# Kernel tuning notes

Hardware: AMD Instinct MI355X
Metric: run time of the kernel (lower is better)

Reference implementation:

```python
import jax, jax.numpy as jnp
import numpy as np

N, M, C, CSKIP, K = 16384, 4096, 256, 128, 3
BIG = 1e10  # distance penalty for cross-batch pairs


def setup_inputs() -> dict:
    key = jax.random.key(0)
    ks = jax.random.split(key, 6)
    return {
        "x": jax.random.normal(ks[0], (M, C), jnp.float32),
        "pos": jax.random.normal(ks[1], (M, 3), jnp.float32),
        "batch": jnp.zeros((M,), jnp.int32),
        "x_skip": jax.random.normal(ks[2], (N, CSKIP), jnp.float32),
        "pos_skip": jax.random.normal(ks[3], (N, 3), jnp.float32),
        "batch_skip": jnp.zeros((N,), jnp.int32),
        "W1": jax.random.normal(ks[4], (C + CSKIP, 256), jnp.float32) * (1.0 / np.sqrt(C + CSKIP)),
        "b1": jnp.zeros((256,), jnp.float32),
        "W2": jax.random.normal(ks[5], (256, 256), jnp.float32) * (1.0 / np.sqrt(256)),
        "b2": jnp.zeros((256,), jnp.float32),
    }


def _knn_idx(pos, pos_skip, batch, batch_skip, k):
    # Squared distances via GEMM form: [N, M]
    a2 = jnp.sum(pos_skip * pos_skip, axis=-1, keepdims=True)      # [N,1]
    b2 = jnp.sum(pos * pos, axis=-1)[None, :]                       # [1,M]
    d2 = a2 + b2 - 2.0 * (pos_skip @ pos.T)                         # [N,M]
    d2 = jnp.where(batch_skip[:, None] != batch[None, :], BIG, d2)
    _, idx = jax.lax.top_k(-d2, k)                                  # [N,k]
    return idx


def reference(x, pos, batch, x_skip, pos_skip, batch_skip, W1, b1, W2, b2):
    idx = _knn_idx(pos, pos_skip, batch, batch_skip, K)             # [N,k] coarse neighbor ids
    # Exact squared dist recomputed from gathered positions (matches torch diff path)
    diff = pos_skip[:, None, :] - pos[idx]                          # [N,k,3]
    d2 = jnp.sum(diff * diff, axis=-1, keepdims=True)               # [N,k,1]
    w = 1.0 / (d2 + 1e-8)                                           # inverse-distance weights
    wsum = jnp.sum(w, axis=1, keepdims=True)                        # per-row scatter_add == sum over k
    w = w / (wsum + 1e-8)
    x_interp = jnp.sum(w * x[idx], axis=1)                          # [N,C]
    h = jnp.concatenate([x_interp, x_skip], axis=1)                 # [N,C+C']
    h = jax.nn.relu(h @ W1 + b1)
    h = jax.nn.relu(h @ W2 + b2)
    return h
```

## Files before the change

### kernel.cpp

```cpp
#include <hip/hip_runtime.h>

typedef float     f4   __attribute__((ext_vector_type(4)));
typedef float     f32x4 __attribute__((ext_vector_type(4)));
typedef _Float16  h8   __attribute__((ext_vector_type(8)));
typedef _Float16  h4   __attribute__((ext_vector_type(4)));
typedef int       i4   __attribute__((ext_vector_type(4)));

#define NQ   16384
#define MP   4096
#define CF   256
#define CSK  128
#define K1   384
#define HID  256
#define QB   16

__global__ __launch_bounds__(256) void wconv_kernel(
    const float* __restrict__ W1, const float* __restrict__ W2,
    _Float16* __restrict__ Wt1, _Float16* __restrict__ Wt2)
{
    const int i = blockIdx.x * 256 + threadIdx.x;
    if (i < K1 * HID) {
        const int k = i >> 8, n = i & 255;
        Wt1[(size_t)(k >> 5) * 8192 + ((k >> 3) & 3) * 2048 + n * 8 + (k & 7)]
            = (_Float16)W1[i];
    } else {
        const int i2 = i - K1 * HID;
        const int k = i2 >> 8, n = i2 & 255;
        Wt2[(size_t)(k >> 5) * 8192 + ((k >> 3) & 3) * 2048 + n * 8 + (k & 7)]
            = (_Float16)W2[i2];
    }
}

__global__ __launch_bounds__(256, 3) void fused_kernel(
    const float* __restrict__ pos,
    const float* __restrict__ pos_skip,
    const float* __restrict__ x,
    const float* __restrict__ x_skip,
    const _Float16* __restrict__ Wt1,
    const _Float16* __restrict__ Wt2,
    const float* __restrict__ b1,
    const float* __restrict__ b2,
    float* __restrict__ out)
{
    __shared__ __align__(16) char smem[51456];
    float* px = (float*)smem;
    float* py = (float*)(smem + 16384);
    float* pz = (float*)(smem + 32768);
    unsigned short (*ci)[48]    = (unsigned short (*)[48])(smem + 49152);
    unsigned short (*ci2)[8][3] = (unsigned short (*)[8][3])(smem + 50688);
    int   (*fidx)[3] = (int (*)[3])(smem + 49152);
    float (*fw)[3]   = (float (*)[3])(smem + 49344);
    _Float16 (*As)[392] = (_Float16 (*)[392])smem;
    _Float16 (*Hs)[264] = (_Float16 (*)[264])smem;

    const int tid = threadIdx.x;

    for (int j = tid; j < MP; j += 256) {
        px[j] = pos[3*j+0];
        py[j] = pos[3*j+1];
        pz[j] = pos[3*j+2];
    }
    __syncthreads();

    const int lane = tid & 63;
    const int wv   = tid >> 6;

    {
        float qx[4], qy[4], qz[4];
        #pragma unroll
        for (int k = 0; k < 4; k++) {
            const int q = blockIdx.x * QB + wv * 4 + k;
            qx[k] = pos_skip[3*q+0];
            qy[k] = pos_skip[3*q+1];
            qz[k] = pos_skip[3*q+2];
        }

        unsigned K0[4], K1v[4], K2[4];
        #pragma unroll
        for (int k = 0; k < 4; k++) { K0[k] = ~0u; K1v[k] = ~0u; K2[k] = ~0u; }

        #define EVAL(PX, PY, PZ, J)                                           \
            _Pragma("unroll")                                                 \
            for (int k = 0; k < 4; k++) {                                     \
                const float dx = qx[k] - (PX), dy = qy[k] - (PY),             \
                            dz = qz[k] - (PZ);                                \
                const float dd = fmaf(dx, dx, fmaf(dy, dy, dz * dz));         \
                const unsigned key = (__float_as_uint(dd) & 0xFFFFF000u) | (J);\
                const unsigned h0 = max(K0[k], key);                          \
                K0[k] = min(K0[k], key);                                      \
                const unsigned n1 = min(K1v[k], h0);                          \
                const unsigned h1 = max(K1v[k], h0);                          \
                K1v[k] = n1;                                                  \
                K2[k] = min(K2[k], h1);                                       \
            }

        float c0x = px[lane],       c1x = px[lane + 64],
              c2x = px[lane + 128], c3x = px[lane + 192];
        float c0y = py[lane],       c1y = py[lane + 64],
              c2y = py[lane + 128], c3y = py[lane + 192];
        float c0z = pz[lane],       c1z = pz[lane + 64],
              c2z = pz[lane + 128], c3z = pz[lane + 192];

        for (int it = 0; it < 64; it += 4) {
            const unsigned jb = it * 64 + lane;
            const float nx0 = px[jb + 256], nx1 = px[jb + 320],
                        nx2 = px[jb + 384], nx3 = px[jb + 448];
            const float ny0 = py[jb + 256], ny1 = py[jb + 320],
                        ny2 = py[jb + 384], ny3 = py[jb + 448];
            const float nz0 = pz[jb + 256], nz1 = pz[jb + 320],
                        nz2 = pz[jb + 384], nz3 = pz[jb + 448];
            EVAL(c0x, c0y, c0z, jb);
            EVAL(c1x, c1y, c1z, jb + 64);
            EVAL(c2x, c2y, c2z, jb + 128);
            EVAL(c3x, c3y, c3z, jb + 192);
            c0x = nx0; c1x = nx1; c2x = nx2; c3x = nx3;
            c0y = ny0; c1y = ny1; c2y = ny2; c3y = ny3;
            c0z = nz0; c1z = nz1; c2z = nz2; c3z = nz3;
        }
        #undef EVAL

        #pragma unroll
        for (int k = 0; k < 4; k++) {
            unsigned a0 = K0[k], a1 = K1v[k], a2 = K2[k];
            {
                const unsigned b0 = (unsigned)__builtin_amdgcn_ds_swizzle((int)a0, 0x041F);
                const unsigned b1 = (unsigned)__builtin_amdgcn_ds_swizzle((int)a1, 0x041F);
                const unsigned b2 = (unsigned)__builtin_amdgcn_ds_swizzle((int)a2, 0x041F);
                const unsigned m0 = min(a0, b0);
                const unsigned c1 = max(a0, b0);
                const unsigned d0 = min(a1, b1), d1 = max(a1, b1);
                const unsigned m1 = min(c1, d0);
                const unsigned m2 = min(min(max(c1, d0), d1), min(a2, b2));
                a0 = m0; a1 = m1; a2 = m2;
            }
            {
                const unsigned b0 = (unsigned)__builtin_amdgcn_ds_swizzle((int)a0, 0x081F);
                const unsigned b1 = (unsigned)__builtin_amdgcn_ds_swizzle((int)a1, 0x081F);
                const unsigned b2 = (unsigned)__builtin_amdgcn_ds_swizzle((int)a2, 0x081F);
                const unsigned m0 = min(a0, b0);
                const unsigned c1 = max(a0, b0);
                const unsigned d0 = min(a1, b1), d1 = max(a1, b1);
                const unsigned m1 = min(c1, d0);
                const unsigned m2 = min(min(max(c1, d0), d1), min(a2, b2));
                a0 = m0; a1 = m1; a2 = m2;
            }
            if (!(lane & 3)) {
                const int q = wv * 4 + k;
                const int pr = lane >> 2;
                ci[q][pr*3+0] = (unsigned short)(a0 & 0xFFFu);
                ci[q][pr*3+1] = (unsigned short)(a1 & 0xFFFu);
                ci[q][pr*3+2] = (unsigned short)(a2 & 0xFFFu);
            }
        }
    }
    __syncthreads();

    if (tid < 8 * QB) {
        const int q    = tid >> 3;
        const int part = tid & 7;
        const int g    = blockIdx.x * QB + q;
        const double qxd = (double)pos_skip[3*g+0];
        const double qyd = (double)pos_skip[3*g+1];
        const double qzd = (double)pos_skip[3*g+2];
        const double a2d = qxd*qxd + qyd*qyd + qzd*qzd;

        double e0 = 1e300, e1 = 1e300, e2 = 1e300;
        int    j0 = 0,     j1 = 0,     j2 = 0;
        #pragma unroll
        for (int c = 0; c < 6; c++) {
            const int j = ci[q][part*6 + c];
            const double pxd = (double)px[j], pyd = (double)py[j],
                         pzd = (double)pz[j];
            const double b2  = pxd*pxd + pyd*pyd + pzd*pzd;
            const double dot = qxd*pxd + qyd*pyd + qzd*pzd;
            const double d   = (a2d + b2) - 2.0 * dot;
            if (d < e2) {
                if (d < e1) {
                    e2 = e1; j2 = j1;
                    if (d < e0) { e1 = e0; j1 = j0; e0 = d; j0 = j; }
                    else        { e1 = d;  j1 = j; }
                } else { e2 = d; j2 = j; }
            }
        }
        ci2[q][part][0] = (unsigned short)j0;
        ci2[q][part][1] = (unsigned short)j1;
        ci2[q][part][2] = (unsigned short)j2;
    }
    __syncthreads();

    if (tid < QB) {
        const int g = blockIdx.x * QB + tid;
        const double qxd = (double)pos_skip[3*g+0];
        const double qyd = (double)pos_skip[3*g+1];
        const double qzd = (double)pos_skip[3*g+2];
        const double a2d = qxd*qxd + qyd*qyd + qzd*qzd;

        double e0 = 1e300, e1 = 1e300, e2 = 1e300;
        int    j0 = 0,     j1 = 0,     j2 = 0;
        for (int p = 0; p < 8; p++) {
            #pragma unroll
            for (int s = 0; s < 3; s++) {
                const int j = ci2[tid][p][s];
                const double pxd = (double)px[j], pyd = (double)py[j],
                             pzd = (double)pz[j];
                const double b2  = pxd*pxd + pyd*pyd + pzd*pzd;
                const double dot = qxd*pxd + qyd*pyd + qzd*pzd;
                const double d   = (a2d + b2) - 2.0 * dot;
                if (d < e2) {
                    if (d < e1) {
                        e2 = e1; j2 = j1;
                        if (d < e0) { e1 = e0; j1 = j0; e0 = d; j0 = j; }
                        else        { e1 = d;  j1 = j; }
                    } else { e2 = d; j2 = j; }
                }
            }
        }
        const float sx = pos_skip[3*g+0], sy = pos_skip[3*g+1], sz = pos_skip[3*g+2];
        const int jj[3] = { j0, j1, j2 };
        float wv3[3];
        #pragma unroll
        for (int k = 0; k < 3; k++) {
            const float dx = sx - px[jj[k]], dy = sy - py[jj[k]],
                        dz = sz - pz[jj[k]];
            const float dd = dx*dx + dy*dy + dz*dz;
            wv3[k] = 1.0f / (dd + 1e-8f);
        }
        const float inv = 1.0f / (wv3[0] + wv3[1] + wv3[2] + 1e-8f);
        #pragma unroll
        for (int k = 0; k < 3; k++) {
            fidx[tid][k] = jj[k];
            fw[tid][k]   = wv3[k] * inv;
        }
    }
    __syncthreads();

    const int row0 = blockIdx.x * QB;

    {
        const int r   = tid >> 4;
        const int sub = tid & 15;
        const int j0 = fidx[r][0], j1 = fidx[r][1], j2 = fidx[r][2];
        const float w0 = fw[r][0], w1 = fw[r][1], w2 = fw[r][2];
        const f4* xa = (const f4*)(x + (size_t)j0 * CF);
        const f4* xb = (const f4*)(x + (size_t)j1 * CF);
        const f4* xc = (const f4*)(x + (size_t)j2 * CF);
        const f4* xs = (const f4*)(x_skip + (size_t)(row0 + r) * CSK);
        #pragma unroll
        for (int t = 0; t < 4; t++) {
            const int c4 = t * 16 + sub;
            const f4 a = xa[c4], b = xb[c4], c = xc[c4];
            const f4 v = a * w0 + b * w1 + c * w2;
            h4 hv; hv[0]=(_Float16)v[0]; hv[1]=(_Float16)v[1];
                   hv[2]=(_Float16)v[2]; hv[3]=(_Float16)v[3];
            *(h4*)&As[r][c4 * 4] = hv;
        }
        #pragma unroll
        for (int t = 0; t < 2; t++) {
            const int c4 = t * 16 + sub;
            const f4 v = xs[c4];
            h4 hv; hv[0]=(_Float16)v[0]; hv[1]=(_Float16)v[1];
                   hv[2]=(_Float16)v[2]; hv[3]=(_Float16)v[3];
            *(h4*)&As[r][CF + c4 * 4] = hv;
        }
    }

    const int ln   = tid & 15;
    const int quad = (tid >> 4) & 3;
    const int nb   = wv * 64;
    const int q8   = quad * 8;

    const _Float16* w1b = Wt1 + quad * 2048 + (size_t)(nb + ln) * 8;
    const _Float16* w2b = Wt2 + quad * 2048 + (size_t)(nb + ln) * 8;

    f32x4 acc[4];
    #pragma unroll
    for (int nt = 0; nt < 4; nt++) acc[nt] = (f32x4)0.0f;

    h8 B[6][4];
    #pragma unroll
    for (int s = 0; s < 6; s++)
        #pragma unroll
        for (int nt = 0; nt < 4; nt++)
            B[s][nt] = *(const h8*)(w1b + (size_t)s * 8192 + nt * 128);

    __syncthreads();

    #pragma unroll
    for (int kb = 0; kb < 12; kb++) {
        const int s = kb % 6;
        const h8 ha = *(const h8*)&As[ln][kb*32 + q8];
        h8 hb[4];
        #pragma unroll
        for (int nt = 0; nt < 4; nt++) hb[nt] = B[s][nt];
        if (kb < 6) {
            #pragma unroll
            for (int nt = 0; nt < 4; nt++)
                B[s][nt] = *(const h8*)(w1b + (size_t)(kb+6) * 8192 + nt * 128);
        } else {
            #pragma unroll
            for (int nt = 0; nt < 4; nt++)
                B[s][nt] = *(const h8*)(w2b + (size_t)(kb-6) * 8192 + nt * 128);
        }
        #pragma unroll
        for (int nt = 0; nt < 4; nt++)
            acc[nt] = __builtin_amdgcn_mfma_f32_16x16x32_f16(ha, hb[nt], acc[nt], 0, 0, 0);
    }
    __syncthreads();

    #pragma unroll
    for (int nt = 0; nt < 4; nt++) {
        const int n = nb + nt*16 + ln;
        const float bv = b1[n];
        #pragma unroll
        for (int r = 0; r < 4; r++) {
            const int m = quad*4 + r;
            Hs[m][n] = (_Float16)fmaxf(acc[nt][r] + bv, 0.0f);
        }
        acc[nt] = (f32x4)0.0f;
    }
    __syncthreads();

    #pragma unroll
    for (int kb = 0; kb < 8; kb++) {
        const int s = kb % 6;
        const h8 ha = *(const h8*)&Hs[ln][kb*32 + q8];
        h8 hb[4];
        #pragma unroll
        for (int nt = 0; nt < 4; nt++) hb[nt] = B[s][nt];
        if (kb < 2) {
            #pragma unroll
            for (int nt = 0; nt < 4; nt++)
                B[s][nt] = *(const h8*)(w2b + (size_t)(kb+6) * 8192 + nt * 128);
        }
        #pragma unroll
        for (int nt = 0; nt < 4; nt++)
            acc[nt] = __builtin_amdgcn_mfma_f32_16x16x32_f16(ha, hb[nt], acc[nt], 0, 0, 0);
    }

    #pragma unroll
    for (int nt = 0; nt < 4; nt++) {
        const int n = nb + nt*16 + ln;
        const float bv = b2[n];
        #pragma unroll
        for (int r = 0; r < 4; r++) {
            const int m = quad*4 + r;
            out[(size_t)(row0 + m) * HID + n] = fmaxf(acc[nt][r] + bv, 0.0f);
        }
    }
}

extern "C" void kernel_launch(void* const* d_in, const int* in_sizes, int n_in,
                              void* d_out, int out_size, void* d_ws, size_t ws_size,
                              hipStream_t stream) {
    const float* x         = (const float*)d_in[0];
    const float* pos       = (const float*)d_in[1];
    const float* x_skip    = (const float*)d_in[3];
    const float* pos_skip  = (const float*)d_in[4];
    const float* W1        = (const float*)d_in[6];
    const float* b1        = (const float*)d_in[7];
    const float* W2        = (const float*)d_in[8];
    const float* b2        = (const float*)d_in[9];
    float* out = (float*)d_out;

    char* ws = (char*)d_ws;
    _Float16* Wt1 = (_Float16*)ws;
    _Float16* Wt2 = (_Float16*)(ws + 196608);

    wconv_kernel<<<(K1*HID + HID*HID) / 256, 256, 0, stream>>>(W1, W2, Wt1, Wt2);
    fused_kernel<<<NQ / QB, 256, 0, stream>>>(pos, pos_skip, x, x_skip,
                                              Wt1, Wt2, b1, b2, out);
}
```

Before: 118.7 us.

## Store candidate positions as fp16 in LDS to double occupancy

Point coordinates are staged in shared memory as fp16 instead of fp32, which halves LDS use to about 26KB. Launch bounds are raised from 3 to 6 blocks per SM to allow more resident blocks. The coarse top-k pass now runs on fp16-rounded coordinates, and the exact double-precision refinement reads full-precision positions from global memory. This risks missing true neighbours if the fp16 error pushes one outside the 48-candidate shortlist, and the tighter register budget may cause spills.

```diff
diff --git a/kernel.cpp b/kernel.cpp
--- a/kernel.cpp
+++ b/kernel.cpp
@@ -31,7 +31,7 @@
     }
 }
 
-__global__ __launch_bounds__(256, 3) void fused_kernel(
+__global__ __launch_bounds__(256, 6) void fused_kernel(
     const float* __restrict__ pos,
     const float* __restrict__ pos_skip,
     const float* __restrict__ x,
@@ -42,23 +42,33 @@
     const float* __restrict__ b2,
     float* __restrict__ out)
 {
-    __shared__ __align__(16) char smem[51456];
-    float* px = (float*)smem;
-    float* py = (float*)(smem + 16384);
-    float* pz = (float*)(smem + 32768);
-    unsigned short (*ci)[48]    = (unsigned short (*)[48])(smem + 49152);
-    unsigned short (*ci2)[8][3] = (unsigned short (*)[8][3])(smem + 50688);
-    int   (*fidx)[3] = (int (*)[3])(smem + 49152);
-    float (*fw)[3]   = (float (*)[3])(smem + 49344);
+    __shared__ __align__(16) char smem[26112];
+    _Float16* pxh = (_Float16*)smem;
+    _Float16* pyh = (_Float16*)(smem + 8192);
+    _Float16* pzh = (_Float16*)(smem + 16384);
+    unsigned short (*ci)[48] = (unsigned short (*)[48])(smem + 24576);
+    int   (*fidx)[3] = (int (*)[3])(smem + 24576);
+    float (*fw)[3]   = (float (*)[3])(smem + 24768);
     _Float16 (*As)[392] = (_Float16 (*)[392])smem;
     _Float16 (*Hs)[264] = (_Float16 (*)[264])smem;
 
     const int tid = threadIdx.x;
 
-    for (int j = tid; j < MP; j += 256) {
-        px[j] = pos[3*j+0];
-        py[j] = pos[3*j+1];
-        pz[j] = pos[3*j+2];
+    {
+        const f4* posv = (const f4*)pos;
+        for (int m = tid; m < MP / 4; m += 256) {
+            const f4 a = posv[3*m], b = posv[3*m+1], c = posv[3*m+2];
+            h4 hx, hy, hz;
+            hx[0]=(_Float16)a[0]; hx[1]=(_Float16)a[3];
+            hx[2]=(_Float16)b[2]; hx[3]=(_Float16)c[1];
+            hy[0]=(_Float16)a[1]; hy[1]=(_Float16)b[0];
+            hy[2]=(_Float16)b[3]; hy[3]=(_Float16)c[2];
+            hz[0]=(_Float16)a[2]; hz[1]=(_Float16)b[1];
+            hz[2]=(_Float16)c[0]; hz[3]=(_Float16)c[3];
+            *(h4*)&pxh[4*m] = hx;
+            *(h4*)&pyh[4*m] = hy;
+            *(h4*)&pzh[4*m] = hz;
+        }
     }
     __syncthreads();
 
@@ -94,21 +104,21 @@
                 K2[k] = min(K2[k], h1);                                       \
             }
 
-        float c0x = px[lane],       c1x = px[lane + 64],
-              c2x = px[lane + 128], c3x = px[lane + 192];
-        float c0y = py[lane],       c1y = py[lane + 64],
-              c2y = py[lane + 128], c3y = py[lane + 192];
-        float c0z = pz[lane],       c1z = pz[lane + 64],
-              c2z = pz[lane + 128], c3z = pz[lane + 192];
+        float c0x = (float)pxh[lane],       c1x = (float)pxh[lane + 64],
+              c2x = (float)pxh[lane + 128], c3x = (float)pxh[lane + 192];
+        float c0y = (float)pyh[lane],       c1y = (float)pyh[lane + 64],
+              c2y = (float)pyh[lane + 128], c3y = (float)pyh[lane + 192];
+        float c0z = (float)pzh[lane],       c1z = (float)pzh[lane + 64],
+              c2z = (float)pzh[lane + 128], c3z = (float)pzh[lane + 192];
 
         for (int it = 0; it < 64; it += 4) {
             const unsigned jb = it * 64 + lane;
-            const float nx0 = px[jb + 256], nx1 = px[jb + 320],
-                        nx2 = px[jb + 384], nx3 = px[jb + 448];
-            const float ny0 = py[jb + 256], ny1 = py[jb + 320],
-                        ny2 = py[jb + 384], ny3 = py[jb + 448];
-            const float nz0 = pz[jb + 256], nz1 = pz[jb + 320],
-                        nz2 = pz[jb + 384], nz3 = pz[jb + 448];
+            const float nx0 = (float)pxh[jb + 256], nx1 = (float)pxh[jb + 320],
+                        nx2 = (float)pxh[jb + 384], nx3 = (float)pxh[jb + 448];
+            const float ny0 = (float)pyh[jb + 256], ny1 = (float)pyh[jb + 320],
+                        ny2 = (float)pyh[jb + 384], ny3 = (float)pyh[jb + 448];
+            const float nz0 = (float)pzh[jb + 256], nz1 = (float)pzh[jb + 320],
+                        nz2 = (float)pzh[jb + 384], nz3 = (float)pzh[jb + 448];
             EVAL(c0x, c0y, c0z, jb);
             EVAL(c1x, c1y, c1z, jb + 64);
             EVAL(c2x, c2y, c2z, jb + 128);
@@ -169,8 +179,9 @@
         #pragma unroll
         for (int c = 0; c < 6; c++) {
             const int j = ci[q][part*6 + c];
-            const double pxd = (double)px[j], pyd = (double)py[j],
-                         pzd = (double)pz[j];
+            const double pxd = (double)pos[3*j+0];
+            const double pyd = (double)pos[3*j+1];
+            const double pzd = (double)pos[3*j+2];
             const double b2  = pxd*pxd + pyd*pyd + pzd*pzd;
             const double dot = qxd*pxd + qyd*pyd + qzd*pzd;
             const double d   = (a2d + b2) - 2.0 * dot;
@@ -182,9 +193,9 @@
                 } else { e2 = d; j2 = j; }
             }
         }
-        ci2[q][part][0] = (unsigned short)j0;
-        ci2[q][part][1] = (unsigned short)j1;
-        ci2[q][part][2] = (unsigned short)j2;
+        ci[q][part*3+0] = (unsigned short)j0;
+        ci[q][part*3+1] = (unsigned short)j1;
+        ci[q][part*3+2] = (unsigned short)j2;
     }
     __syncthreads();
 
@@ -200,9 +211,10 @@
         for (int p = 0; p < 8; p++) {
             #pragma unroll
             for (int s = 0; s < 3; s++) {
-                const int j = ci2[tid][p][s];
-                const double pxd = (double)px[j], pyd = (double)py[j],
-                             pzd = (double)pz[j];
+                const int j = ci[tid][p*3+s];
+                const double pxd = (double)pos[3*j+0];
+                const double pyd = (double)pos[3*j+1];
+                const double pzd = (double)pos[3*j+2];
                 const double b2  = pxd*pxd + pyd*pyd + pzd*pzd;
                 const double dot = qxd*pxd + qyd*pyd + qzd*pzd;
                 const double d   = (a2d + b2) - 2.0 * dot;
@@ -220,8 +232,9 @@
         float wv3[3];
         #pragma unroll
         for (int k = 0; k < 3; k++) {
-            const float dx = sx - px[jj[k]], dy = sy - py[jj[k]],
-                        dz = sz - pz[jj[k]];
+            const float dx = sx - pos[3*jj[k]+0];
+            const float dy = sy - pos[3*jj[k]+1];
+            const float dz = sz - pos[3*jj[k]+2];
             const float dd = dx*dx + dy*dy + dz*dz;
             wv3[k] = 1.0f / (dd + 1e-8f);
         }
```

New measurement: 150.8 us. +27.0%, slower.
